# Kernel optimization log

Measured on AMD Instinct MI355X. Metric: run time of the kernel, lower is better.

The kernel has to match this reference:

```python
import jax, jax.numpy as jnp
import numpy as np

MASK_ATTENTION = 10000000000.0
PAD_IDX = 0


def setup_inputs() -> dict:
    key = jax.random.key(0)
    ks = jax.random.split(key, 12)
    S, T, B, H, V = 256, 64, 8, 768, 50257
    return {
        "encoder_out": jax.random.normal(ks[0], (S, B, H), dtype=jnp.float32),
        "decoder_state": jax.random.normal(ks[1], (T, B, H), dtype=jnp.float32),
        "src_ids": jax.random.randint(ks[2], (S, B), 0, V, dtype=jnp.int64),
        "tgt_embedding": jax.random.normal(ks[3], (T, B, H), dtype=jnp.float32),
        "W_attn": jax.random.normal(ks[4], (2 * H, H), dtype=jnp.float32) * 0.02,
        "b_attn": jax.random.normal(ks[5], (H,), dtype=jnp.float32) * 0.02,
        "v_attn": jax.random.normal(ks[6], (H,), dtype=jnp.float32) * 0.02,
        "b_v": jax.random.normal(ks[7], (1,), dtype=jnp.float32) * 0.02,
        "W_pgen": jax.random.normal(ks[8], (3 * H, 1), dtype=jnp.float32) * 0.02,
        "b_pgen": jax.random.normal(ks[9], (1,), dtype=jnp.float32) * 0.02,
        "W_gen": jax.random.normal(ks[10], (H, V), dtype=jnp.float32) * 0.02,
        "b_gen": jax.random.normal(ks[11], (V,), dtype=jnp.float32) * 0.02,
    }


def reference(encoder_out, decoder_state, src_ids, tgt_embedding,
              W_attn, b_attn, v_attn, b_v, W_pgen, b_pgen, W_gen, b_gen):
    # encoder_out: [S,B,H], decoder_state/tgt_embedding: [T,B,H], src_ids: [S,B]
    T, B, H = decoder_state.shape
    S = encoder_out.shape[0]
    # Split the cat+Linear into two projections (same math as Linear on concat)
    Wd, We = W_attn[:H], W_attn[H:]
    dec_proj = decoder_state @ Wd                     # [T,B,H]
    enc_proj = encoder_out @ We + b_attn              # [S,B,H]
    energy = jnp.tanh(dec_proj[:, None] + enc_proj[None])  # [T,S,B,H]
    attention = energy @ v_attn + b_v[0]              # [T,S,B]
    pad_mask = (src_ids == PAD_IDX)                   # [S,B]
    attn_dist = jnp.where(pad_mask[None], -MASK_ATTENTION, attention)
    attn_prob = jax.nn.softmax(attn_dist, axis=1)     # softmax over S: [T,S,B]
    ctx = jnp.einsum('tsb,sbh->tbh', attn_prob, encoder_out)  # [T,B,H]
    p_gen_input = jnp.concatenate((decoder_state, ctx, tgt_embedding), axis=2)
    p_gen = jax.nn.sigmoid(p_gen_input @ W_pgen + b_pgen)     # [T,B,1]
    vocab_prob = jax.nn.softmax(decoder_state @ W_gen + b_gen, axis=2)  # [T,B,V]
    vocab_prob_ = vocab_prob * p_gen
    attn_prob_ = jnp.transpose(attn_prob, (0, 2, 1)) * (1.0 - p_gen)    # [T,B,S]
    idx = jnp.broadcast_to(src_ids.T[None], (T, B, S))                  # [T,B,S]
    ti = jnp.arange(T)[:, None, None]
    bi = jnp.arange(B)[None, :, None]
    final_prob = vocab_prob_.at[ti, bi, idx].add(attn_prob_)
    return final_prob


if __name__ == "__main__":
    out = reference(**setup_inputs())
    print(out.shape)
```

## Files before the change

### kernel.cpp

```cpp
#include <hip/hip_runtime.h>
#include <stdint.h>

#define S_ 256
#define T_ 64
#define B_ 8
#define H_ 768
#define V_ 50257
#define R_ 512
#define VP_ 50304
#define NBLK_ 393
#define NBP_ 400

typedef __attribute__((ext_vector_type(8))) short short8;
typedef __attribute__((ext_vector_type(4))) float float4v;

__device__ __forceinline__ float bf2f(unsigned short u) {
  union { unsigned int i; float f; } x; x.i = ((unsigned int)u) << 16; return x.f;
}
__device__ __forceinline__ short f2bf(float f) {
  union { float f; unsigned int i; } x; x.f = f;
  unsigned int u = x.i;
  unsigned int r = u + 0x7fffu + ((u >> 16) & 1u);
  return (short)(r >> 16);
}
__device__ __forceinline__ float tanh_fast(float x) {
  float e = __builtin_amdgcn_exp2f(2.885390082f * x);
  float r = __builtin_amdgcn_rcpf(e + 1.f);
  return fmaf(-2.f, r, 1.f);
}
__device__ __forceinline__ void gload16(const short* g, short* l) {
  __builtin_amdgcn_global_load_lds(
      (const __attribute__((address_space(1))) unsigned int*)g,
      (__attribute__((address_space(3))) unsigned int*)l, 16, 0, 0);
}
__device__ __forceinline__ int swz(int r, int c) {
  return r * 64 + (c ^ ((r & 7) * 8));
}

__global__ __launch_bounds__(256) void cvt_kernel(const float* __restrict__ dec,
                                                  const float* __restrict__ enc,
                                                  short* __restrict__ dec16,
                                                  short* __restrict__ enc16, float* rowsums) {
  int tid = blockIdx.x * 256 + threadIdx.x;
  if (tid < R_) rowsums[tid] = 0.f;
  const int nd4 = R_ * H_ / 4;
  const float4v* src;
  short* dst;
  int off;
  if (tid < nd4) { src = (const float4v*)dec; dst = dec16; off = tid; }
  else           { src = (const float4v*)enc; dst = enc16; off = tid - nd4; }
  float4v v = src[off];
  union { short s[4]; unsigned long long u; } pk;
  pk.s[0] = f2bf(v[0]); pk.s[1] = f2bf(v[1]); pk.s[2] = f2bf(v[2]); pk.s[3] = f2bf(v[3]);
  *(unsigned long long*)&dst[(size_t)off * 4] = pk.u;
}

__global__ __launch_bounds__(256) void twat_kernel(const float* in, short* out) {
  __shared__ float tile[64][65];
  int n0 = blockIdx.x * 64;
  int k0 = blockIdx.y * 64;
  int t = threadIdx.x;
  int c = t & 63, rsub = t >> 6;
#pragma unroll
  for (int i = 0; i < 16; ++i) {
    int r = i * 4 + rsub;
    tile[r][c] = in[(size_t)(k0 + r) * 768 + n0 + c];
  }
  __syncthreads();
#pragma unroll
  for (int i = 0; i < 16; ++i) {
    int nn = i * 4 + rsub;
    out[(size_t)(n0 + nn) * 1536 + k0 + c] = f2bf(tile[c][nn]);
  }
}

__global__ __launch_bounds__(256) void cvt_wt_kernel(const float* __restrict__ in,
                                                     short* __restrict__ out) {
  __shared__ float tile[64][133];
  int v0 = blockIdx.x * 128;
  int k0 = blockIdx.y * 64;
  int t = threadIdx.x;
  int lc = t & 127, lr2 = t >> 7;
#pragma unroll
  for (int p = 0; p < 32; ++p) {
    int r = p * 2 + lr2;
    int v = v0 + lc;
    tile[r][lc] = (v < V_) ? in[(size_t)(k0 + r) * V_ + v] : 0.f;
  }
  __syncthreads();
  int kg = t & 7, vsub = t >> 3;
#pragma unroll
  for (int p = 0; p < 4; ++p) {
    int vv = p * 32 + vsub;
    union { short s[8]; short8 v8; } pk;
#pragma unroll
    for (int j = 0; j < 8; ++j) pk.s[j] = f2bf(tile[kg * 8 + j][vv]);
    *(short8*)&out[(size_t)(v0 + vv) * 768 + k0 + kg * 8] = pk.v8;
  }
}

__global__ __launch_bounds__(256, 3) void gemm_proj(const short* __restrict__ A,
                                                    const short* __restrict__ BT,
                                                    int koff, const float* __restrict__ bias,
                                                    float* __restrict__ C) {
  __shared__ __align__(16) short Bl[2][128 * 64];
  int t = threadIdx.x;
  int w = t >> 6, l = t & 63;
  int n0 = blockIdx.x * 128;
  int m0 = blockIdx.y * 128;
  int wm = w >> 1, wn = w & 1;
  int lm = l & 15, lq = l >> 4;
  int srow = t >> 3;
  int scol = ((t & 7) ^ (srow & 7)) * 8;

  float4v acc[4][4];
#pragma unroll
  for (int i = 0; i < 4; ++i)
#pragma unroll
    for (int j = 0; j < 4; ++j) acc[i][j] = float4v{0.f, 0.f, 0.f, 0.f};

  const short* bS = BT + (size_t)(n0 + srow) * 1536 + koff + scol;
  const short* aR = A + (size_t)(m0 + wm * 64 + lm) * 768 + lq * 8;

  auto STAGE = [&](int buf, int kk) {
#pragma unroll
    for (int i = 0; i < 4; ++i)
      gload16(bS + (size_t)i * 32 * 1536 + kk, &Bl[buf][(i * 32 + w * 8) * 64]);
  };

  STAGE(0, 0);
#pragma unroll 1
  for (int kt = 0; kt < 12; ++kt) {
    int cb = kt & 1;
    int kk = kt * 64;
    short8 af[2][4];
#pragma unroll
    for (int ks = 0; ks < 2; ++ks)
#pragma unroll
      for (int mt = 0; mt < 4; ++mt)
        af[ks][mt] = *(const short8*)&aR[(size_t)mt * 16 * 768 + kk + ks * 32];
    if (kt < 11) {
      STAGE(cb ^ 1, kk + 64);
      asm volatile("s_waitcnt vmcnt(12)" ::: "memory");
    } else {
      asm volatile("s_waitcnt vmcnt(8)" ::: "memory");
    }
    __builtin_amdgcn_s_barrier();

    short8 bfr[2][4];
#pragma unroll
    for (int ks = 0; ks < 2; ++ks)
#pragma unroll
      for (int nt = 0; nt < 4; ++nt)
        bfr[ks][nt] = *(const short8*)&Bl[cb][swz(wn * 64 + nt * 16 + lm, ks * 32 + lq * 8)];
    asm volatile("s_waitcnt lgkmcnt(0)" ::: "memory");
    if (kt < 11)
      asm volatile("s_waitcnt vmcnt(4)" ::: "memory");
    else
      asm volatile("s_waitcnt vmcnt(0)" ::: "memory");
    __builtin_amdgcn_s_barrier();

#pragma unroll
    for (int ks = 0; ks < 2; ++ks)
#pragma unroll
      for (int mt = 0; mt < 4; ++mt)
#pragma unroll
        for (int nt = 0; nt < 4; ++nt)
          acc[mt][nt] = __builtin_amdgcn_mfma_f32_16x16x32_bf16(af[ks][mt], bfr[ks][nt],
                                                                acc[mt][nt], 0, 0, 0);
  }

  int q4 = lq * 4, ln = lm;
#pragma unroll
  for (int nt = 0; nt < 4; ++nt) {
    int c = n0 + wn * 64 + nt * 16 + ln;
    float bv = bias ? bias[c] : 0.f;
#pragma unroll
    for (int mt = 0; mt < 4; ++mt)
#pragma unroll
      for (int r = 0; r < 4; ++r)
        C[(size_t)(m0 + wm * 64 + mt * 16 + q4 + r) * 768 + c] = acc[mt][nt][r] + bv;
  }
}

__global__ __launch_bounds__(256) void energy_kernel(const float* __restrict__ dproj,
                                                     const float* __restrict__ eproj,
                                                     const float* vattn, const float* bv,
                                                     float* scores) {
  __shared__ float dch[16][65];
  __shared__ float ech[16][65];
  __shared__ float vch[64];
  int s0 = blockIdx.x * 16;
  int b  = blockIdx.y;
  int t0 = blockIdx.z * 16;
  int t = threadIdx.x;
  int sl = t & 15, tl = t >> 4;
  float acc = 0.f;
  for (int hc = 0; hc < 768; hc += 64) {
#pragma unroll
    for (int i = 0; i < 4; ++i) {
      int idx = i * 256 + t;
      int rr = idx >> 6, cc = idx & 63;
      dch[rr][cc] = dproj[(size_t)((t0 + rr) * 8 + b) * 768 + hc + cc];
      ech[rr][cc] = eproj[(size_t)((s0 + rr) * 8 + b) * 768 + hc + cc];
    }
    if (t < 64) vch[t] = vattn[hc + t];
    __syncthreads();
#pragma unroll 8
    for (int hh = 0; hh < 64; ++hh) {
      float x = dch[tl][hh] + ech[sl][hh];
      acc = fmaf(tanh_fast(x), vch[hh], acc);
    }
    __syncthreads();
  }
  scores[(size_t)((t0 + tl) * 8 + b) * 256 + s0 + sl] = acc + bv[0];
}

__global__ __launch_bounds__(256) void softmax_kernel(const float* scores, const int* sid, float* P) {
  __shared__ float red[256];
  int r = blockIdx.x, t = threadIdx.x, b = r & 7;
  float v = scores[(size_t)r * 256 + t];
  if (sid[t * 8 + b] == 0) v = -1e10f;
  red[t] = v;
  __syncthreads();
  for (int s = 128; s > 0; s >>= 1) {
    if (t < s) red[t] = fmaxf(red[t], red[t + s]);
    __syncthreads();
  }
  float m = red[0];
  __syncthreads();
  float e = __expf(v - m);
  red[t] = e;
  __syncthreads();
  for (int s = 128; s > 0; s >>= 1) {
    if (t < s) red[t] += red[t + s];
    __syncthreads();
  }
  P[(size_t)r * 256 + t] = e * (1.f / red[0]);
}

__global__ __launch_bounds__(256) void ctx_kernel(const float* __restrict__ P,
                                                  const float* __restrict__ enc, float* ctx) {
  __shared__ float Pl[16][256];
  int h0 = blockIdx.x * 64;
  int b  = blockIdx.y;
  int tg = blockIdx.z;
  int t = threadIdx.x;
  int hl = t & 63, wv = t >> 6;
#pragma unroll
  for (int i = 0; i < 16; ++i) {
    int idx = i * 256 + t;
    int tt = idx >> 8, s = idx & 255;
    Pl[tt][s] = P[(size_t)((tg * 16 + tt) * 8 + b) * 256 + s];
  }
  __syncthreads();
  float acc[4] = {0.f, 0.f, 0.f, 0.f};
#pragma unroll 4
  for (int s = 0; s < 256; ++s) {
    float e = enc[(size_t)(s * 8 + b) * 768 + h0 + hl];
#pragma unroll
    for (int j = 0; j < 4; ++j)
      acc[j] = fmaf(Pl[wv * 4 + j][s], e, acc[j]);
  }
#pragma unroll
  for (int j = 0; j < 4; ++j)
    ctx[(size_t)((tg * 16 + wv * 4 + j) * 8 + b) * 768 + h0 + hl] = acc[j];
}

__global__ __launch_bounds__(256) void pgen_kernel(const float* dec, const float* ctx,
                                                   const float* tgt, const float* Wp,
                                                   const float* bp, float* pgen) {
  __shared__ float red[256];
  int r = blockIdx.x, t = threadIdx.x;
  float s = 0.f;
  for (int h = t; h < 768; h += 256) {
    s = fmaf(dec[(size_t)r * 768 + h], Wp[h], s);
    s = fmaf(ctx[(size_t)r * 768 + h], Wp[768 + h], s);
    s = fmaf(tgt[(size_t)r * 768 + h], Wp[1536 + h], s);
  }
  red[t] = s;
  __syncthreads();
  for (int st = 128; st > 0; st >>= 1) {
    if (t < st) red[t] += red[t + st];
    __syncthreads();
  }
  if (t == 0) pgen[r] = 1.f / (1.f + __expf(-(red[0] + bp[0])));
}

__global__ __launch_bounds__(256, 3) void gemm_vocab(const short* __restrict__ A,
                                                     const short* __restrict__ BT,
                                                     const float* __restrict__ bgen,
                                                     short* __restrict__ E,
                                                     float* __restrict__ prs) {
  __shared__ __align__(16) short Bl[2][128 * 64];
  int t = threadIdx.x;
  int w = t >> 6, l = t & 63;
  int orig = blockIdx.x;
  int xcd = orig & 7, ix = orig >> 3;
  int wgid = (xcd < 4 ? xcd * 197 : 788 + (xcd - 4) * 196) + ix;
  int n0 = (wgid >> 2) * 128;
  int m0 = (wgid & 3) * 128;
  int nblk = wgid >> 2;
  int wm = w >> 1, wn = w & 1;
  int lm = l & 15, lq = l >> 4;
  int srow = t >> 3;
  int scol = ((t & 7) ^ (srow & 7)) * 8;

  float4v acc[4][4];
#pragma unroll
  for (int i = 0; i < 4; ++i)
#pragma unroll
    for (int j = 0; j < 4; ++j) acc[i][j] = float4v{0.f, 0.f, 0.f, 0.f};

  const short* bS = BT + (size_t)(n0 + srow) * 768 + scol;
  const short* aR = A + (size_t)(m0 + wm * 64 + lm) * 768 + lq * 8;

  auto STAGE = [&](int buf, int kk) {
#pragma unroll
    for (int i = 0; i < 4; ++i)
      gload16(bS + (size_t)i * 32 * 768 + kk, &Bl[buf][(i * 32 + w * 8) * 64]);
  };

  STAGE(0, 0);
#pragma unroll 1
  for (int kt = 0; kt < 12; ++kt) {
    int cb = kt & 1;
    int kk = kt * 64;
    short8 af[2][4];
#pragma unroll
    for (int ks = 0; ks < 2; ++ks)
#pragma unroll
      for (int mt = 0; mt < 4; ++mt)
        af[ks][mt] = *(const short8*)&aR[(size_t)mt * 16 * 768 + kk + ks * 32];
    if (kt < 11) {
      STAGE(cb ^ 1, kk + 64);
      asm volatile("s_waitcnt vmcnt(12)" ::: "memory");
    } else {
      asm volatile("s_waitcnt vmcnt(8)" ::: "memory");
    }
    __builtin_amdgcn_s_barrier();

    short8 bfr[2][4];
#pragma unroll
    for (int ks = 0; ks < 2; ++ks)
#pragma unroll
      for (int nt = 0; nt < 4; ++nt)
        bfr[ks][nt] = *(const short8*)&Bl[cb][swz(wn * 64 + nt * 16 + lm, ks * 32 + lq * 8)];
    asm volatile("s_waitcnt lgkmcnt(0)" ::: "memory");
    if (kt < 11)
      asm volatile("s_waitcnt vmcnt(4)" ::: "memory");
    else
      asm volatile("s_waitcnt vmcnt(0)" ::: "memory");
    __builtin_amdgcn_s_barrier();

#pragma unroll
    for (int ks = 0; ks < 2; ++ks)
#pragma unroll
      for (int mt = 0; mt < 4; ++mt)
#pragma unroll
        for (int nt = 0; nt < 4; ++nt)
          acc[mt][nt] = __builtin_amdgcn_mfma_f32_16x16x32_bf16(af[ks][mt], bfr[ks][nt],
                                                                acc[mt][nt], 0, 0, 0);
  }

  int q4 = lq * 4, ln = lm;
  float rs[4][4];
#pragma unroll
  for (int i = 0; i < 4; ++i)
#pragma unroll
    for (int j = 0; j < 4; ++j) rs[i][j] = 0.f;
#pragma unroll
  for (int nt = 0; nt < 4; ++nt) {
    int c = n0 + wn * 64 + nt * 16 + ln;
    bool valid = c < V_;
    float bg = valid ? bgen[c] : 0.f;
#pragma unroll
    for (int mt = 0; mt < 4; ++mt)
#pragma unroll
      for (int r = 0; r < 4; ++r) {
        float e = valid ? __expf(acc[mt][nt][r] + bg) : 0.f;
        int row = m0 + wm * 64 + mt * 16 + q4 + r;
        E[(size_t)row * VP_ + c] = f2bf(e);
        rs[mt][r] += e;
      }
  }
  float* red = (float*)Bl;
  if (t < 128) red[t] = 0.f;
  __syncthreads();
#pragma unroll
  for (int mt = 0; mt < 4; ++mt)
#pragma unroll
    for (int r = 0; r < 4; ++r) {
      float v = rs[mt][r];
      v += __shfl_xor(v, 1);
      v += __shfl_xor(v, 2);
      v += __shfl_xor(v, 4);
      v += __shfl_xor(v, 8);
      if (ln == 0) atomicAdd(&red[wm * 64 + mt * 16 + q4 + r], v);
    }
  __syncthreads();
  if (t < 128) prs[(size_t)(m0 + t) * NBP_ + nblk] = red[t];
}

__global__ __launch_bounds__(256) void rowsum_reduce(const float* __restrict__ prs,
                                                     float* __restrict__ rowsums) {
  __shared__ float red[256];
  int r = blockIdx.x, t = threadIdx.x;
  float s = prs[(size_t)r * NBP_ + t];
  if (t + 256 < NBLK_) s += prs[(size_t)r * NBP_ + t + 256];
  red[t] = s;
  __syncthreads();
  for (int st = 128; st > 0; st >>= 1) {
    if (t < st) red[t] += red[t + st];
    __syncthreads();
  }
  if (t == 0) rowsums[r] = red[0];
}

__global__ __launch_bounds__(256) void final_kernel(const short* __restrict__ E,
                                                    const float* __restrict__ P,
                                                    const float* pgen, const float* rowsums,
                                                    const int* sid, float* __restrict__ out) {
  int r = blockIdx.y, t = threadIdx.x, b = r & 7;
  int lo = blockIdx.x * 2048, hi = lo + 2048;
  float pg = pgen[r];
  float scale = pg / rowsums[r];
  const short* Er = E + (size_t)r * VP_;
  float* outr = out + (size_t)r * V_;
#pragma unroll
  for (int j = 0; j < 8; ++j) {
    int c = lo + j * 256 + t;
    if (c < V_) outr[c] = bf2f((unsigned short)Er[c]) * scale;
  }
  __syncthreads();
  int idx = sid[t * 8 + b];
  if (idx >= lo && idx < hi) {
    float ap = (1.f - pg) * P[(size_t)r * 256 + t];
    atomicAdd(&outr[idx], ap);
  }
}

extern "C" void kernel_launch(void* const* d_in, const int* in_sizes, int n_in,
                              void* d_out, int out_size, void* d_ws, size_t ws_size,
                              hipStream_t stream) {
  const float* enc  = (const float*)d_in[0];
  const float* dec  = (const float*)d_in[1];
  const int*   sid  = (const int*)d_in[2];
  const float* tgt  = (const float*)d_in[3];
  const float* Wat  = (const float*)d_in[4];
  const float* batt = (const float*)d_in[5];
  const float* vatt = (const float*)d_in[6];
  const float* bv   = (const float*)d_in[7];
  const float* Wp   = (const float*)d_in[8];
  const float* bp   = (const float*)d_in[9];
  const float* Wg   = (const float*)d_in[10];
  const float* bg   = (const float*)d_in[11];
  float* out = (float*)d_out;

  char* ws = (char*)d_ws;
  size_t off = 0;
  auto alloc = [&](size_t bytes) -> char* {
    char* p = ws + off;
    off += (bytes + 255) & ~(size_t)255;
    return p;
  };
  short* E16     = (short*)alloc((size_t)R_ * VP_ * 2);
  short* WT16    = (short*)alloc((size_t)VP_ * H_ * 2);
  short* dec16   = (short*)alloc((size_t)R_ * H_ * 2);
  short* enc16   = (short*)alloc((size_t)S_ * B_ * H_ * 2);
  short* WAT16   = (short*)alloc((size_t)H_ * 1536 * 2);
  float* dproj   = (float*)alloc((size_t)R_ * H_ * 4);
  float* eproj   = (float*)alloc((size_t)S_ * B_ * H_ * 4);
  float* scores  = (float*)alloc((size_t)R_ * 256 * 4);
  float* P       = (float*)alloc((size_t)R_ * 256 * 4);
  float* ctx     = (float*)alloc((size_t)R_ * H_ * 4);
  float* pgen    = (float*)alloc(R_ * 4);
  float* rowsums = (float*)alloc(R_ * 4);
  float* prs     = (float*)alloc((size_t)R_ * NBP_ * 4);

  cvt_kernel<<<1920, 256, 0, stream>>>(dec, enc, dec16, enc16, rowsums);
  twat_kernel<<<dim3(12, 24), 256, 0, stream>>>(Wat, WAT16);
  cvt_wt_kernel<<<dim3(393, 12), 256, 0, stream>>>(Wg, WT16);
  gemm_proj<<<dim3(6, 4), 256, 0, stream>>>(dec16, WAT16, 0, nullptr, dproj);
  gemm_proj<<<dim3(6, 16), 256, 0, stream>>>(enc16, WAT16, 768, batt, eproj);
  energy_kernel<<<dim3(16, 8, 4), 256, 0, stream>>>(dproj, eproj, vatt, bv, scores);
  softmax_kernel<<<512, 256, 0, stream>>>(scores, sid, P);
  ctx_kernel<<<dim3(12, 8, 4), 256, 0, stream>>>(P, enc, ctx);
  pgen_kernel<<<512, 256, 0, stream>>>(dec, ctx, tgt, Wp, bp, pgen);
  gemm_vocab<<<dim3(1572), 256, 0, stream>>>(dec16, WT16, bg, E16, prs);
  rowsum_reduce<<<512, 256, 0, stream>>>(prs, rowsums);
  final_kernel<<<dim3(25, 512), 256, 0, stream>>>(E16, P, pgen, rowsums, sid, out);
}
```

Before: 586.2 us.

## Split vocab GEMM into double- and single-buffered halves; retile weight conversion

The vocabulary GEMM is split into two launches. The first covers half the column blocks and keeps the double-buffered LDS pipeline at 3 blocks per CU. The second covers the rest with single-buffered LDS and a launch bound of 6 blocks per CU, aiming for higher occupancy. The W_gen transpose/convert kernel now uses larger 512x32 tiles stored as bf16 in LDS, which halves LDS use and batches the global loads. The trade-off is an extra launch, and the single-buffered half loses load/compute overlap.

```diff
diff --git a/kernel.cpp b/kernel.cpp
--- a/kernel.cpp
+++ b/kernel.cpp
@@ -76,26 +76,37 @@
 
 __global__ __launch_bounds__(256) void cvt_wt_kernel(const float* __restrict__ in,
                                                      short* __restrict__ out) {
-  __shared__ float tile[64][133];
-  int v0 = blockIdx.x * 128;
-  int k0 = blockIdx.y * 64;
+  __shared__ short tile[32][522];
+  int v0 = blockIdx.x * 512, k0 = blockIdx.y * 32;
   int t = threadIdx.x;
-  int lc = t & 127, lr2 = t >> 7;
-#pragma unroll
-  for (int p = 0; p < 32; ++p) {
-    int r = p * 2 + lr2;
-    int v = v0 + lc;
-    tile[r][lc] = (v < V_) ? in[(size_t)(k0 + r) * V_ + v] : 0.f;
-  }
-  __syncthreads();
-  int kg = t & 7, vsub = t >> 3;
-#pragma unroll
-  for (int p = 0; p < 4; ++p) {
-    int vv = p * 32 + vsub;
-    union { short s[8]; short8 v8; } pk;
-#pragma unroll
-    for (int j = 0; j < 8; ++j) pk.s[j] = f2bf(tile[kg * 8 + j][vv]);
-    *(short8*)&out[(size_t)(v0 + vv) * 768 + k0 + kg * 8] = pk.v8;
+#pragma unroll
+  for (int g = 0; g < 4; ++g) {
+    float vals[16];
+#pragma unroll
+    for (int i = 0; i < 16; ++i) {
+      int q = (g * 16 + i) * 256 + t;
+      int r = q >> 9, c = q & 511;
+      int v = v0 + c;
+      vals[i] = (v < V_) ? in[(size_t)(k0 + r) * V_ + v] : 0.f;
+    }
+#pragma unroll
+    for (int i = 0; i < 16; ++i) {
+      int q = (g * 16 + i) * 256 + t;
+      tile[q >> 9][q & 511] = f2bf(vals[i]);
+    }
+  }
+  __syncthreads();
+  int kq = t & 3, vs = t >> 2;
+#pragma unroll
+  for (int p = 0; p < 8; ++p) {
+    int vv = p * 64 + vs;
+    int vrow = v0 + vv;
+    if (vrow < VP_) {
+      union { short s[8]; short8 v8; } pk;
+#pragma unroll
+      for (int j = 0; j < 8; ++j) pk.s[j] = tile[kq * 8 + j][vv];
+      *(short8*)&out[(size_t)vrow * 768 + k0 + kq * 8] = pk.v8;
+    }
   }
 }
 
@@ -287,20 +298,20 @@
   if (t == 0) pgen[r] = 1.f / (1.f + __expf(-(red[0] + bp[0])));
 }
 
-__global__ __launch_bounds__(256, 3) void gemm_vocab(const short* __restrict__ A,
-                                                     const short* __restrict__ BT,
-                                                     const float* __restrict__ bgen,
-                                                     short* __restrict__ E,
-                                                     float* __restrict__ prs) {
+__global__ __launch_bounds__(256, 3) void gemm_vocab_a(const short* __restrict__ A,
+                                                       const short* __restrict__ BT,
+                                                       const float* __restrict__ bgen,
+                                                       short* __restrict__ E,
+                                                       float* __restrict__ prs) {
   __shared__ __align__(16) short Bl[2][128 * 64];
   int t = threadIdx.x;
   int w = t >> 6, l = t & 63;
   int orig = blockIdx.x;
   int xcd = orig & 7, ix = orig >> 3;
-  int wgid = (xcd < 4 ? xcd * 197 : 788 + (xcd - 4) * 196) + ix;
-  int n0 = (wgid >> 2) * 128;
+  int wgid = (xcd < 4 ? xcd * 99 : 396 + (xcd - 4) * 98) + ix;
+  int nblk = wgid >> 2;
+  int n0 = nblk * 128;
   int m0 = (wgid & 3) * 128;
-  int nblk = wgid >> 2;
   int wm = w >> 1, wn = w & 1;
   int lm = l & 15, lq = l >> 4;
   int srow = t >> 3;
@@ -351,6 +362,106 @@
       asm volatile("s_waitcnt vmcnt(4)" ::: "memory");
     else
       asm volatile("s_waitcnt vmcnt(0)" ::: "memory");
+    __builtin_amdgcn_s_barrier();
+
+#pragma unroll
+    for (int ks = 0; ks < 2; ++ks)
+#pragma unroll
+      for (int mt = 0; mt < 4; ++mt)
+#pragma unroll
+        for (int nt = 0; nt < 4; ++nt)
+          acc[mt][nt] = __builtin_amdgcn_mfma_f32_16x16x32_bf16(af[ks][mt], bfr[ks][nt],
+                                                                acc[mt][nt], 0, 0, 0);
+  }
+
+  int q4 = lq * 4, ln = lm;
+  float rs[4][4];
+#pragma unroll
+  for (int i = 0; i < 4; ++i)
+#pragma unroll
+    for (int j = 0; j < 4; ++j) rs[i][j] = 0.f;
+#pragma unroll
+  for (int nt = 0; nt < 4; ++nt) {
+    int c = n0 + wn * 64 + nt * 16 + ln;
+    bool valid = c < V_;
+    float bg = valid ? bgen[c] : 0.f;
+#pragma unroll
+    for (int mt = 0; mt < 4; ++mt)
+#pragma unroll
+      for (int r = 0; r < 4; ++r) {
+        float e = valid ? __expf(acc[mt][nt][r] + bg) : 0.f;
+        int row = m0 + wm * 64 + mt * 16 + q4 + r;
+        E[(size_t)row * VP_ + c] = f2bf(e);
+        rs[mt][r] += e;
+      }
+  }
+  float* red = (float*)Bl;
+  if (t < 128) red[t] = 0.f;
+  __syncthreads();
+#pragma unroll
+  for (int mt = 0; mt < 4; ++mt)
+#pragma unroll
+    for (int r = 0; r < 4; ++r) {
+      float v = rs[mt][r];
+      v += __shfl_xor(v, 1);
+      v += __shfl_xor(v, 2);
+      v += __shfl_xor(v, 4);
+      v += __shfl_xor(v, 8);
+      if (ln == 0) atomicAdd(&red[wm * 64 + mt * 16 + q4 + r], v);
+    }
+  __syncthreads();
+  if (t < 128) prs[(size_t)(m0 + t) * NBP_ + nblk] = red[t];
+}
+
+__global__ __launch_bounds__(256, 6) void gemm_vocab_b(const short* __restrict__ A,
+                                                       const short* __restrict__ BT,
+                                                       const float* __restrict__ bgen,
+                                                       short* __restrict__ E,
+                                                       float* __restrict__ prs) {
+  __shared__ __align__(16) short Bl[128 * 64];
+  int t = threadIdx.x;
+  int w = t >> 6, l = t & 63;
+  int orig = blockIdx.x;
+  int wgid = (orig & 7) * 98 + (orig >> 3);
+  int nblk = 197 + (wgid >> 2);
+  int n0 = nblk * 128;
+  int m0 = (wgid & 3) * 128;
+  int wm = w >> 1, wn = w & 1;
+  int lm = l & 15, lq = l >> 4;
+  int srow = t >> 3;
+  int scol = ((t & 7) ^ (srow & 7)) * 8;
+
+  float4v acc[4][4];
+#pragma unroll
+  for (int i = 0; i < 4; ++i)
+#pragma unroll
+    for (int j = 0; j < 4; ++j) acc[i][j] = float4v{0.f, 0.f, 0.f, 0.f};
+
+  const short* bS = BT + (size_t)(n0 + srow) * 768 + scol;
+  const short* aR = A + (size_t)(m0 + wm * 64 + lm) * 768 + lq * 8;
+
+#pragma unroll 1
+  for (int kt = 0; kt < 12; ++kt) {
+    int kk = kt * 64;
+    short8 af[2][4];
+#pragma unroll
+    for (int ks = 0; ks < 2; ++ks)
+#pragma unroll
+      for (int mt = 0; mt < 4; ++mt)
+        af[ks][mt] = *(const short8*)&aR[(size_t)mt * 16 * 768 + kk + ks * 32];
+#pragma unroll
+    for (int i = 0; i < 4; ++i)
+      gload16(bS + (size_t)i * 32 * 768 + kk, &Bl[(i * 32 + w * 8) * 64]);
+    asm volatile("s_waitcnt vmcnt(0)" ::: "memory");
+    __builtin_amdgcn_s_barrier();
+
+    short8 bfr[2][4];
+#pragma unroll
+    for (int ks = 0; ks < 2; ++ks)
+#pragma unroll
+      for (int nt = 0; nt < 4; ++nt)
+        bfr[ks][nt] = *(const short8*)&Bl[swz(wn * 64 + nt * 16 + lm, ks * 32 + lq * 8)];
+    asm volatile("s_waitcnt lgkmcnt(0)" ::: "memory");
     __builtin_amdgcn_s_barrier();
 
 #pragma unroll
@@ -480,14 +591,15 @@
 
   cvt_kernel<<<1920, 256, 0, stream>>>(dec, enc, dec16, enc16, rowsums);
   twat_kernel<<<dim3(12, 24), 256, 0, stream>>>(Wat, WAT16);
-  cvt_wt_kernel<<<dim3(393, 12), 256, 0, stream>>>(Wg, WT16);
+  cvt_wt_kernel<<<dim3(99, 24), 256, 0, stream>>>(Wg, WT16);
   gemm_proj<<<dim3(6, 4), 256, 0, stream>>>(dec16, WAT16, 0, nullptr, dproj);
   gemm_proj<<<dim3(6, 16), 256, 0, stream>>>(enc16, WAT16, 768, batt, eproj);
   energy_kernel<<<dim3(16, 8, 4), 256, 0, stream>>>(dproj, eproj, vatt, bv, scores);
   softmax_kernel<<<512, 256, 0, stream>>>(scores, sid, P);
   ctx_kernel<<<dim3(12, 8, 4), 256, 0, stream>>>(P, enc, ctx);
   pgen_kernel<<<512, 256, 0, stream>>>(dec, ctx, tgt, Wp, bp, pgen);
-  gemm_vocab<<<dim3(1572), 256, 0, stream>>>(dec16, WT16, bg, E16, prs);
+  gemm_vocab_a<<<dim3(788), 256, 0, stream>>>(dec16, WT16, bg, E16, prs);
+  gemm_vocab_b<<<dim3(784), 256, 0, stream>>>(dec16, WT16, bg, E16, prs);
   rowsum_reduce<<<512, 256, 0, stream>>>(prs, rowsums);
   final_kernel<<<dim3(25, 512), 256, 0, stream>>>(E16, P, pgen, rowsums, sid, out);
 }
```

New measurement: 765.4 us. +30.6%, slower.

## Triple-buffer vocab GEMM B tiles and widen weight-transpose conversion tiles

Applied to the files above, without the earlier changes.

The vocab GEMM moves from a double-buffered LDS pipeline to a fully unrolled triple-buffered one. B tiles are prefetched two k-steps ahead and A fragments one step ahead, using ping-pong registers, with occupancy lowered from 3 to 2 blocks. The W_gen transpose/convert kernel now stages 32x512 bf16 tiles in LDS instead of 64x128 float tiles, which batches global loads and halves LDS footprint per element. In exchange there is more register and LDS pressure and lower occupancy in the GEMM.

```diff
diff --git a/kernel.cpp b/kernel.cpp
--- a/kernel.cpp
+++ b/kernel.cpp
@@ -76,26 +76,37 @@
 
 __global__ __launch_bounds__(256) void cvt_wt_kernel(const float* __restrict__ in,
                                                      short* __restrict__ out) {
-  __shared__ float tile[64][133];
-  int v0 = blockIdx.x * 128;
-  int k0 = blockIdx.y * 64;
+  __shared__ short tile[32][522];
+  int v0 = blockIdx.x * 512, k0 = blockIdx.y * 32;
   int t = threadIdx.x;
-  int lc = t & 127, lr2 = t >> 7;
-#pragma unroll
-  for (int p = 0; p < 32; ++p) {
-    int r = p * 2 + lr2;
-    int v = v0 + lc;
-    tile[r][lc] = (v < V_) ? in[(size_t)(k0 + r) * V_ + v] : 0.f;
-  }
-  __syncthreads();
-  int kg = t & 7, vsub = t >> 3;
-#pragma unroll
-  for (int p = 0; p < 4; ++p) {
-    int vv = p * 32 + vsub;
-    union { short s[8]; short8 v8; } pk;
-#pragma unroll
-    for (int j = 0; j < 8; ++j) pk.s[j] = f2bf(tile[kg * 8 + j][vv]);
-    *(short8*)&out[(size_t)(v0 + vv) * 768 + k0 + kg * 8] = pk.v8;
+#pragma unroll
+  for (int g = 0; g < 4; ++g) {
+    float vals[16];
+#pragma unroll
+    for (int i = 0; i < 16; ++i) {
+      int q = (g * 16 + i) * 256 + t;
+      int r = q >> 9, c = q & 511;
+      int v = v0 + c;
+      vals[i] = (v < V_) ? in[(size_t)(k0 + r) * V_ + v] : 0.f;
+    }
+#pragma unroll
+    for (int i = 0; i < 16; ++i) {
+      int q = (g * 16 + i) * 256 + t;
+      tile[q >> 9][q & 511] = f2bf(vals[i]);
+    }
+  }
+  __syncthreads();
+  int kq = t & 3, vs = t >> 2;
+#pragma unroll
+  for (int p = 0; p < 8; ++p) {
+    int vv = p * 64 + vs;
+    int vrow = v0 + vv;
+    if (vrow < VP_) {
+      union { short s[8]; short8 v8; } pk;
+#pragma unroll
+      for (int j = 0; j < 8; ++j) pk.s[j] = tile[kq * 8 + j][vv];
+      *(short8*)&out[(size_t)vrow * 768 + k0 + kq * 8] = pk.v8;
+    }
   }
 }
 
@@ -287,20 +298,20 @@
   if (t == 0) pgen[r] = 1.f / (1.f + __expf(-(red[0] + bp[0])));
 }
 
-__global__ __launch_bounds__(256, 3) void gemm_vocab(const short* __restrict__ A,
+__global__ __launch_bounds__(256, 2) void gemm_vocab(const short* __restrict__ A,
                                                      const short* __restrict__ BT,
                                                      const float* __restrict__ bgen,
                                                      short* __restrict__ E,
                                                      float* __restrict__ prs) {
-  __shared__ __align__(16) short Bl[2][128 * 64];
+  __shared__ __align__(16) short Bl[3][128 * 64];
   int t = threadIdx.x;
   int w = t >> 6, l = t & 63;
   int orig = blockIdx.x;
   int xcd = orig & 7, ix = orig >> 3;
   int wgid = (xcd < 4 ? xcd * 197 : 788 + (xcd - 4) * 196) + ix;
-  int n0 = (wgid >> 2) * 128;
+  int nblk = wgid >> 2;
+  int n0 = nblk * 128;
   int m0 = (wgid & 3) * 128;
-  int nblk = wgid >> 2;
   int wm = w >> 1, wn = w & 1;
   int lm = l & 15, lq = l >> 4;
   int srow = t >> 3;
@@ -315,53 +326,76 @@
   const short* bS = BT + (size_t)(n0 + srow) * 768 + scol;
   const short* aR = A + (size_t)(m0 + wm * 64 + lm) * 768 + lq * 8;
 
-  auto STAGE = [&](int buf, int kk) {
-#pragma unroll
-    for (int i = 0; i < 4; ++i)
-      gload16(bS + (size_t)i * 32 * 768 + kk, &Bl[buf][(i * 32 + w * 8) * 64]);
-  };
-
-  STAGE(0, 0);
-#pragma unroll 1
-  for (int kt = 0; kt < 12; ++kt) {
-    int cb = kt & 1;
-    int kk = kt * 64;
-    short8 af[2][4];
-#pragma unroll
-    for (int ks = 0; ks < 2; ++ks)
-#pragma unroll
-      for (int mt = 0; mt < 4; ++mt)
-        af[ks][mt] = *(const short8*)&aR[(size_t)mt * 16 * 768 + kk + ks * 32];
-    if (kt < 11) {
-      STAGE(cb ^ 1, kk + 64);
-      asm volatile("s_waitcnt vmcnt(12)" ::: "memory");
-    } else {
-      asm volatile("s_waitcnt vmcnt(8)" ::: "memory");
-    }
-    __builtin_amdgcn_s_barrier();
-
-    short8 bfr[2][4];
-#pragma unroll
-    for (int ks = 0; ks < 2; ++ks)
-#pragma unroll
-      for (int nt = 0; nt < 4; ++nt)
-        bfr[ks][nt] = *(const short8*)&Bl[cb][swz(wn * 64 + nt * 16 + lm, ks * 32 + lq * 8)];
-    asm volatile("s_waitcnt lgkmcnt(0)" ::: "memory");
-    if (kt < 11)
-      asm volatile("s_waitcnt vmcnt(4)" ::: "memory");
-    else
-      asm volatile("s_waitcnt vmcnt(0)" ::: "memory");
-    __builtin_amdgcn_s_barrier();
-
-#pragma unroll
-    for (int ks = 0; ks < 2; ++ks)
-#pragma unroll
-      for (int mt = 0; mt < 4; ++mt)
-#pragma unroll
-        for (int nt = 0; nt < 4; ++nt)
-          acc[mt][nt] = __builtin_amdgcn_mfma_f32_16x16x32_bf16(af[ks][mt], bfr[ks][nt],
-                                                                acc[mt][nt], 0, 0, 0);
-  }
+  short8 afA[2][4], afB[2][4];
+
+#define STAGE_V(buf, kt_)                                                      \
+  {                                                                            \
+    _Pragma("unroll")                                                          \
+    for (int i_ = 0; i_ < 4; ++i_)                                             \
+      gload16(bS + (size_t)i_ * 32 * 768 + (kt_) * 64,                         \
+              &Bl[buf][(i_ * 32 + w * 8) * 64]);                               \
+  }
+#define LOADA_V(dst, kt_)                                                      \
+  {                                                                            \
+    _Pragma("unroll")                                                          \
+    for (int ks_ = 0; ks_ < 2; ++ks_)                                          \
+      _Pragma("unroll")                                                        \
+      for (int mt_ = 0; mt_ < 4; ++mt_)                                        \
+        dst[ks_][mt_] = *(const short8*)&aR[(size_t)mt_ * 16 * 768 +           \
+                                            (kt_) * 64 + ks_ * 32];            \
+  }
+#define PHASE_V(kt, AFcur, AFnxt)                                              \
+  {                                                                            \
+    if ((kt) + 1 < 12) LOADA_V(AFnxt, (kt) + 1);                               \
+    if ((kt) + 2 < 12) STAGE_V(((kt) + 2) % 3, (kt) + 2);                      \
+    if ((kt) + 2 < 12)                                                         \
+      asm volatile("s_waitcnt vmcnt(16)" ::: "memory");                        \
+    else if ((kt) + 1 < 12)                                                    \
+      asm volatile("s_waitcnt vmcnt(12)" ::: "memory");                        \
+    else                                                                       \
+      asm volatile("s_waitcnt vmcnt(0)" ::: "memory");                         \
+    __builtin_amdgcn_s_barrier();                                              \
+    __builtin_amdgcn_sched_barrier(0);                                         \
+    short8 bfr[2][4];                                                          \
+    _Pragma("unroll")                                                          \
+    for (int ks_ = 0; ks_ < 2; ++ks_)                                          \
+      _Pragma("unroll")                                                        \
+      for (int nt_ = 0; nt_ < 4; ++nt_)                                        \
+        bfr[ks_][nt_] = *(const short8*)&Bl[(kt) % 3]                          \
+            [swz(wn * 64 + nt_ * 16 + lm, ks_ * 32 + lq * 8)];                 \
+    asm volatile("s_waitcnt lgkmcnt(0)" ::: "memory");                         \
+    __builtin_amdgcn_sched_barrier(0);                                         \
+    __builtin_amdgcn_s_barrier();                                              \
+    _Pragma("unroll")                                                          \
+    for (int ks_ = 0; ks_ < 2; ++ks_)                                          \
+      _Pragma("unroll")                                                        \
+      for (int mt_ = 0; mt_ < 4; ++mt_)                                        \
+        _Pragma("unroll")                                                      \
+        for (int nt_ = 0; nt_ < 4; ++nt_)                                      \
+          acc[mt_][nt_] = __builtin_amdgcn_mfma_f32_16x16x32_bf16(             \
+              AFcur[ks_][mt_], bfr[ks_][nt_], acc[mt_][nt_], 0, 0, 0);         \
+  }
+
+  STAGE_V(0, 0);
+  LOADA_V(afA, 0);
+  STAGE_V(1, 1);
+
+  PHASE_V(0, afA, afB)
+  PHASE_V(1, afB, afA)
+  PHASE_V(2, afA, afB)
+  PHASE_V(3, afB, afA)
+  PHASE_V(4, afA, afB)
+  PHASE_V(5, afB, afA)
+  PHASE_V(6, afA, afB)
+  PHASE_V(7, afB, afA)
+  PHASE_V(8, afA, afB)
+  PHASE_V(9, afB, afA)
+  PHASE_V(10, afA, afB)
+  PHASE_V(11, afB, afA)
+
+#undef PHASE_V
+#undef LOADA_V
+#undef STAGE_V
 
   int q4 = lq * 4, ln = lm;
   float rs[4][4];
@@ -480,7 +514,7 @@
 
   cvt_kernel<<<1920, 256, 0, stream>>>(dec, enc, dec16, enc16, rowsums);
   twat_kernel<<<dim3(12, 24), 256, 0, stream>>>(Wat, WAT16);
-  cvt_wt_kernel<<<dim3(393, 12), 256, 0, stream>>>(Wg, WT16);
+  cvt_wt_kernel<<<dim3(99, 24), 256, 0, stream>>>(Wg, WT16);
   gemm_proj<<<dim3(6, 4), 256, 0, stream>>>(dec16, WAT16, 0, nullptr, dproj);
   gemm_proj<<<dim3(6, 16), 256, 0, stream>>>(enc16, WAT16, 768, batt, eproj);
   energy_kernel<<<dim3(16, 8, 4), 256, 0, stream>>>(dproj, eproj, vatt, bv, scores);
```

New measurement: 547.4 us. -6.6%, faster.
